# Kernel tuning notes

Hardware: AMD Instinct MI355X
Metric: run time of the kernel (lower is better)

Reference implementation:

```python
import jax, jax.numpy as jnp
import numpy as np

H = 16       # num_attention_heads
KV = 4       # num_key_value_heads
HD = 128     # head_dim
BASE = 10000.0


def rotate_half(x):
    x1, x2 = jnp.split(x, 2, axis=-1)
    return jnp.concatenate((-x2, x1), axis=-1)


def rope_cos_sin(position_ids):
    # inv_freq: (HD/2,)
    inv_freq = 1.0 / (BASE ** (jnp.arange(0, HD, 2, dtype=jnp.float32) / HD))
    freqs = position_ids.astype(jnp.float32)[..., None] * inv_freq  # (B, S, HD/2)
    emb = jnp.concatenate((freqs, freqs), axis=-1)  # (B, S, HD)
    return jnp.cos(emb), jnp.sin(emb)


def setup_inputs() -> dict:
    key = jax.random.key(0)
    ks = jax.random.split(key, 5)
    B, S, D = 2, 2048, 2048
    sc = 1.0 / np.sqrt(D)
    return {
        "hidden_states": jax.random.normal(ks[0], (B, S, D), jnp.float32),
        "position_ids": jnp.broadcast_to(jnp.arange(S, dtype=jnp.int32), (B, S)),
        "wq": jax.random.normal(ks[1], (H * HD, D), jnp.float32) * sc,
        "wk": jax.random.normal(ks[2], (KV * HD, D), jnp.float32) * sc,
        "wv": jax.random.normal(ks[3], (KV * HD, D), jnp.float32) * sc,
        "wo": jax.random.normal(ks[4], (H * HD, H * HD), jnp.float32) * sc,
    }


def attention_forward(hidden_states, position_ids, wq, wk, wv, wo):
    B, S, D = hidden_states.shape
    n_rep = H // KV
    # projections -> (B, heads, S, HD)
    q = (hidden_states @ wq.T).reshape(B, S, H, HD).transpose(0, 2, 1, 3)
    k = (hidden_states @ wk.T).reshape(B, S, KV, HD).transpose(0, 2, 1, 3)
    v = (hidden_states @ wv.T).reshape(B, S, KV, HD).transpose(0, 2, 1, 3)
    # RoPE
    cos, sin = rope_cos_sin(position_ids)  # (B, S, HD)
    cos = cos[:, None]  # (B, 1, S, HD)
    sin = sin[:, None]
    q = q * cos + rotate_half(q) * sin
    k = k * cos + rotate_half(k) * sin
    # repeat kv heads for GQA: (B, KV, S, HD) -> (B, H, S, HD)
    k = jnp.repeat(k, n_rep, axis=1)
    v = jnp.repeat(v, n_rep, axis=1)
    scale = 1.0 / np.sqrt(HD)
    scores = jnp.einsum("bhqd,bhkd->bhqk", q, k) * scale
    attn = jax.nn.softmax(scores.astype(jnp.float32), axis=-1).astype(q.dtype)
    out = jnp.einsum("bhqk,bhkd->bhqd", attn, v)
    out = out.transpose(0, 2, 1, 3).reshape(B, S, H * HD)
    return out @ wo.T


def reference(hidden_states, position_ids, wq, wk, wv, wo):
    return attention_forward(hidden_states, position_ids, wq, wk, wv, wo)
```

## Files before the change

### kernel.cpp

```cpp
#include <hip/hip_runtime.h>
#include <hip/hip_bf16.h>
#include <math.h>


typedef __attribute__((ext_vector_type(4))) float f32x4;
typedef __attribute__((ext_vector_type(8))) short short8;
typedef __attribute__((ext_vector_type(4))) unsigned short u16x4;
typedef __attribute__((ext_vector_type(8))) unsigned short u16x8;

static __device__ __forceinline__ unsigned short f2bf(float x) {
    unsigned u = __builtin_bit_cast(unsigned, x);
    u += 0x7fffu + ((u >> 16) & 1u);
    return (unsigned short)(u >> 16);
}
static __device__ __forceinline__ float bf2f(unsigned short h) {
    unsigned u = ((unsigned)h) << 16;
    return __builtin_bit_cast(float, u);
}
static __device__ __forceinline__ float exp2_fast(float x) {
    float r;
    asm volatile("v_exp_f32 %0, %1" : "=v"(r) : "v"(x));
    return r;
}
static __device__ __forceinline__ void gload16(const unsigned short* g, unsigned short* lds) {
    __builtin_amdgcn_global_load_lds((const __attribute__((address_space(1))) void*)g,
                                     (__attribute__((address_space(3))) void*)lds, 16, 0, 0);
}

__global__ __launch_bounds__(256) void k_conv(const float* __restrict__ src,
                                              unsigned short* __restrict__ dst, int n4) {
    int i = blockIdx.x * 256 + threadIdx.x;
    if (i >= n4) return;
    f32x4 v = ((const f32x4*)src)[i];
    u16x4 o;
    o.x = f2bf(v.x); o.y = f2bf(v.y); o.z = f2bf(v.z); o.w = f2bf(v.w);
    ((u16x4*)dst)[i] = o;
}

__global__ __launch_bounds__(256) void k_conv_wqkv(const float* __restrict__ wq,
                                                   const float* __restrict__ wk,
                                                   const float* __restrict__ wv,
                                                   unsigned short* __restrict__ dst) {
    int i = blockIdx.x * 256 + threadIdx.x;
    long flat = (long)i * 4;
    int row = (int)(flat >> 11);
    int col = (int)(flat & 2047);
    const float* src;
    if (row < 2560) {
        int base = row & 2047;
        int hh = base >> 7, ii = base & 127;
        int d = (ii >> 1) + ((ii & 1) << 6);
        src = (row < 2048 ? wq : wk) + (size_t)(hh * 128 + d) * 2048;
    } else {
        src = wv + (size_t)(row - 2560) * 2048;
    }
    f32x4 v = *(const f32x4*)(src + col);
    u16x4 o;
    o.x = f2bf(v.x); o.y = f2bf(v.y); o.z = f2bf(v.z); o.w = f2bf(v.w);
    *(u16x4*)(dst + flat) = o;
}

__global__ void k_rope_table(const int* __restrict__ pos_ids, float2* __restrict__ tb) {
    int r = blockIdx.x;
    int i = threadIdx.x;
    float pos = (float)pos_ids[r];
    float powv = (float)pow(10000.0, (double)i / 64.0);
    float invf = 1.0f / powv;
    float arg  = pos * invf;
    double a = (double)arg;
    tb[(size_t)r * 64 + i] = make_float2((float)cos(a), (float)sin(a));
}

template <int EPI>
__global__ __launch_bounds__(256) void k_gemm(const unsigned short* __restrict__ A,
                                              const unsigned short* __restrict__ W,
                                              float* __restrict__ Cf,
                                              unsigned short* __restrict__ qkvt,
                                              unsigned short* __restrict__ vtb,
                                              const float2* __restrict__ tb,
                                              int M, int N, int K) {
    __shared__ unsigned short As[2][4096];
    __shared__ unsigned short Ws[2][4096];
    const int tid = threadIdx.x;
    const int lane = tid & 63;
    const int w = tid >> 6;
    const int q = lane & 15, g = lane >> 4;
    const int wr = w >> 1, wc = w & 1;
    const long mbase = (long)blockIdx.y * 128;
    const long nbase = (long)blockIdx.x * 128;

    const unsigned short* gA[2];
    const unsigned short* gW[2];
    #pragma unroll
    for (int j = 0; j < 2; ++j) {
        int r = j * 64 + (tid >> 2);
        int slot = (tid & 3) ^ ((r >> 1) & 3);
        gA[j] = A + (size_t)(mbase + r) * K + slot * 8;
        gW[j] = W + (size_t)(nbase + r) * K + slot * 8;
    }
    const int sa = (g ^ ((q >> 1) & 3)) * 8;

    f32x4 acc[4][4];
    #pragma unroll
    for (int m = 0; m < 4; ++m)
        #pragma unroll
        for (int n = 0; n < 4; ++n) acc[m][n] = (f32x4){0.f, 0.f, 0.f, 0.f};

    auto STAGE = [&](int buf) {
        #pragma unroll
        for (int j = 0; j < 2; ++j) {
            gload16(gA[j], &As[buf][j * 2048 + w * 512]);
            gload16(gW[j], &Ws[buf][j * 2048 + w * 512]);
            gA[j] += 32; gW[j] += 32;
        }
    };

    const int nk = K >> 5;
    STAGE(0);
    int cur = 0;
    for (int t = 0; t < nk; ++t) {
        if (t) __builtin_amdgcn_s_barrier();
        if (t + 1 < nk) {
            STAGE(cur ^ 1);
            asm volatile("s_waitcnt vmcnt(4)" ::: "memory");
        } else {
            asm volatile("s_waitcnt vmcnt(0)" ::: "memory");
        }
        __builtin_amdgcn_s_barrier();

        short8 af[4], bfr[4];
        #pragma unroll
        for (int m = 0; m < 4; ++m) af[m] = *(const short8*)&As[cur][(wr * 64 + m * 16 + q) * 32 + sa];
        #pragma unroll
        for (int n = 0; n < 4; ++n) bfr[n] = *(const short8*)&Ws[cur][(wc * 64 + n * 16 + q) * 32 + sa];
        #pragma unroll
        for (int m = 0; m < 4; ++m)
            #pragma unroll
            for (int n = 0; n < 4; ++n)
                acc[m][n] = __builtin_amdgcn_mfma_f32_16x16x32_bf16(af[m], bfr[n], acc[m][n], 0, 0, 0);
        cur ^= 1;
    }

    if (EPI == 0) {
        #pragma unroll
        for (int m = 0; m < 4; ++m)
            #pragma unroll
            for (int n = 0; n < 4; ++n)
                #pragma unroll
                for (int rr = 0; rr < 4; ++rr) {
                    long row = mbase + wr * 64 + m * 16 + 4 * g + rr;
                    long col = nbase + wc * 64 + n * 16 + q;
                    Cf[row * N + col] = acc[m][n][rr];
                }
    } else {
        const int tile = blockIdx.x;
        if (tile >= 20) {
            const int kv = tile - 20;
            #pragma unroll
            for (int m = 0; m < 4; ++m)
                #pragma unroll
                for (int n = 0; n < 4; ++n) {
                    int c = wc * 64 + n * 16 + q;
                    long r0 = mbase + wr * 64 + m * 16 + 4 * g;
                    int b = (int)(r0 >> 11), s0 = (int)(r0 & 2047);
                    u16x4 pk;
                    #pragma unroll
                    for (int rr = 0; rr < 4; ++rr) pk[rr] = f2bf(acc[m][n][rr]);
                    *(u16x4*)(vtb + (size_t)((b * 4 + kv) * 128 + c) * 2048 + s0) = pk;
                }
        } else {
            const float scale = (tile < 16) ? 0.12751744f : 1.0f;
            const float sgn = (q & 1) ? 1.f : -1.f;
            #pragma unroll
            for (int m = 0; m < 4; ++m)
                #pragma unroll
                for (int rr = 0; rr < 4; ++rr) {
                    long row = mbase + wr * 64 + m * 16 + 4 * g + rr;
                    #pragma unroll
                    for (int n = 0; n < 4; ++n) {
                        int c = wc * 64 + n * 16 + q;
                        float x = acc[m][n][rr];
                        float p = __shfl_xor(x, 1);
                        float2 cs = tb[row * 64 + (c >> 1)];
                        float y = (x * cs.x + sgn * (p * cs.y)) * scale;
                        int dorig = (c >> 1) + ((c & 1) << 6);
                        long col = (tile < 16) ? (tile * 128 + dorig)
                                               : (2048 + (tile - 16) * 128 + dorig);
                        qkvt[row * 3072 + col] = f2bf(y);
                    }
                }
        }
    }
}

__global__ __launch_bounds__(256, 2) void k_flash(const unsigned short* __restrict__ qkv,
                                                  const unsigned short* __restrict__ vt,
                                                  unsigned short* __restrict__ aout) {
    __shared__ unsigned short Ks[2][8192];
    __shared__ unsigned short Vs[2][8192];
    __shared__ unsigned short Plds[4][1152];
    const int wg = blockIdx.x;
    const int kvg = wg & 7;
    const int inner = wg >> 3;
    const int h_in = inner & 3;
    const int qt = inner >> 2;
    const int b = kvg >> 2, kvh = kvg & 3;
    const int h = kvh * 4 + h_in;
    const int tid = threadIdx.x;
    const int w = tid >> 6, lane = tid & 63;
    const int q = lane & 15, g = lane >> 4;
    const int qrow = qt * 128 + w * 32;

    short8 qf[2][4];
    #pragma unroll
    for (int u = 0; u < 2; ++u) {
        const unsigned short* Qp = qkv + (size_t)(b * 2048 + qrow + u * 16 + q) * 3072 + h * 128 + g * 8;
        #pragma unroll
        for (int t = 0; t < 4; ++t) qf[u][t] = *(const short8*)(Qp + t * 32);
    }

    const unsigned short* Kbase = qkv + (size_t)(b * 2048) * 3072 + 2048 + kvh * 128;
    const unsigned short* Vbase = vt + (size_t)((b * 4 + kvh) * 128) * 2048;
    const unsigned short* gK[4];
    const unsigned short* gV[4];
    #pragma unroll
    for (int i = 0; i < 4; ++i) {
        int rowK = w * 16 + i * 4 + (lane >> 4);
        gK[i] = Kbase + (size_t)rowK * 3072 + (((lane & 15) ^ (rowK & 7)) << 3);
        int rowV = w * 32 + i * 8 + (lane >> 3);
        gV[i] = Vbase + (size_t)rowV * 2048 + (((lane & 7) ^ (rowV & 7)) << 3);
    }

    const int swz = (q & 7) << 3;
    int tcK[4];
    #pragma unroll
    for (int t = 0; t < 4; ++t) tcK[t] = (t * 32 + g * 8) ^ swz;

    unsigned short* Pw = Plds[w];

    float m_run[2] = {-INFINITY, -INFINITY};
    float l_run[2] = {0.f, 0.f};
    f32x4 o[2][8];
    #pragma unroll
    for (int u = 0; u < 2; ++u)
        #pragma unroll
        for (int nf = 0; nf < 8; ++nf) o[u][nf] = (f32x4){0.f, 0.f, 0.f, 0.f};

    auto STAGE = [&](int buf) {
        #pragma unroll
        for (int i = 0; i < 4; ++i) {
            gload16(gK[i], &Ks[buf][w * 2048 + i * 512]);
            gload16(gV[i], &Vs[buf][w * 2048 + i * 512]);
            gK[i] += 64 * 3072;
            gV[i] += 64;
        }
    };

    STAGE(0);
    int cur = 0;
    for (int t0 = 0; t0 < 32; ++t0) {
        if (t0 > 0) __builtin_amdgcn_s_barrier();
        if (t0 + 1 < 32) {
            STAGE(cur ^ 1);
            asm volatile("s_waitcnt vmcnt(8)" ::: "memory");
        } else {
            asm volatile("s_waitcnt vmcnt(0)" ::: "memory");
        }
        __builtin_amdgcn_s_barrier();

        const unsigned short* Kt = Ks[cur];
        const unsigned short* Vt = Vs[cur];

        f32x4 st[2][4];
        #pragma unroll
        for (int ks = 0; ks < 4; ++ks) {
            f32x4 a0 = (f32x4){0.f, 0.f, 0.f, 0.f};
            f32x4 a1 = (f32x4){0.f, 0.f, 0.f, 0.f};
            int rb = (ks * 16 + q) * 128;
            #pragma unroll
            for (int t = 0; t < 4; ++t) {
                short8 kf = *(const short8*)&Kt[rb + tcK[t]];
                a0 = __builtin_amdgcn_mfma_f32_16x16x32_bf16(kf, qf[0][t], a0, 0, 0, 0);
                a1 = __builtin_amdgcn_mfma_f32_16x16x32_bf16(kf, qf[1][t], a1, 0, 0, 0);
            }
            st[0][ks] = a0; st[1][ks] = a1;
        }

        short8 vf[8][2];
        #pragma unroll
        for (int nf = 0; nf < 8; ++nf) {
            int rb = (nf * 16 + q) * 64;
            #pragma unroll
            for (int t = 0; t < 2; ++t) vf[nf][t] = *(const short8*)&Vt[rb + tcK[t]];
        }

        #pragma unroll
        for (int u = 0; u < 2; ++u) {
            float mx = fmaxf(
                fmaxf(fmaxf(fmaxf(st[u][0][0], st[u][0][1]), fmaxf(st[u][0][2], st[u][0][3])),
                      fmaxf(fmaxf(st[u][1][0], st[u][1][1]), fmaxf(st[u][1][2], st[u][1][3]))),
                fmaxf(fmaxf(fmaxf(st[u][2][0], st[u][2][1]), fmaxf(st[u][2][2], st[u][2][3])),
                      fmaxf(fmaxf(st[u][3][0], st[u][3][1]), fmaxf(st[u][3][2], st[u][3][3]))));
            mx = fmaxf(mx, __shfl_xor(mx, 16));
            mx = fmaxf(mx, __shfl_xor(mx, 32));
            if (__any(mx - m_run[u] > 8.0f)) {
                float mn = fmaxf(m_run[u], mx);
                float sc = exp2_fast(m_run[u] - mn);
                l_run[u] *= sc;
                f32x4 sv;
                #pragma unroll
                for (int rr = 0; rr < 4; ++rr) sv[rr] = __shfl(sc, 4 * g + rr);
                #pragma unroll
                for (int nf = 0; nf < 8; ++nf) o[u][nf] *= sv;
                m_run[u] = mn;
            }
            f32x4 pe[4];
            #pragma unroll
            for (int ks = 0; ks < 4; ++ks)
                #pragma unroll
                for (int rr = 0; rr < 4; ++rr) pe[ks][rr] = exp2_fast(st[u][ks][rr] - m_run[u]);
            f32x4 ls4 = (pe[0] + pe[1]) + (pe[2] + pe[3]);
            float ls = (ls4[0] + ls4[1]) + (ls4[2] + ls4[3]);
            ls += __shfl_xor(ls, 16);
            ls += __shfl_xor(ls, 32);
            l_run[u] += ls;

            #pragma unroll
            for (int ks = 0; ks < 4; ++ks) {
                u16x4 pk;
                #pragma unroll
                for (int rr = 0; rr < 4; ++rr) pk[rr] = f2bf(pe[ks][rr]);
                *(u16x4*)&Pw[q * 72 + ks * 16 + 4 * g] = pk;
            }
            asm volatile("s_waitcnt lgkmcnt(0)" ::: "memory");
            short8 pa0 = *(const short8*)&Pw[q * 72 + g * 8];
            short8 pa1 = *(const short8*)&Pw[q * 72 + 32 + g * 8];

            #pragma unroll
            for (int nf = 0; nf < 8; ++nf) {
                f32x4 a = o[u][nf];
                a = __builtin_amdgcn_mfma_f32_16x16x32_bf16(pa0, vf[nf][0], a, 0, 0, 0);
                a = __builtin_amdgcn_mfma_f32_16x16x32_bf16(pa1, vf[nf][1], a, 0, 0, 0);
                o[u][nf] = a;
            }
        }
        cur ^= 1;
    }

    #pragma unroll
    for (int u = 0; u < 2; ++u) {
        f32x4 li;
        #pragma unroll
        for (int rr = 0; rr < 4; ++rr) li[rr] = __shfl(l_run[u], 4 * g + rr);
        #pragma unroll
        for (int nf = 0; nf < 8; ++nf)
            #pragma unroll
            for (int rr = 0; rr < 4; ++rr) {
                size_t row = (size_t)(b * 2048 + qrow + u * 16 + 4 * g + rr);
                aout[row * 2048 + h * 128 + nf * 16 + q] = f2bf(o[u][nf][rr] / li[rr]);
            }
    }
}

extern "C" void kernel_launch(void* const* d_in, const int* in_sizes, int n_in,
                              void* d_out, int out_size, void* d_ws, size_t ws_size,
                              hipStream_t stream) {
    (void)in_sizes; (void)n_in; (void)out_size; (void)ws_size;
    const float* hs = (const float*)d_in[0];
    const int* pos  = (const int*)d_in[1];
    const float* wq = (const float*)d_in[2];
    const float* wk = (const float*)d_in[3];
    const float* wv = (const float*)d_in[4];
    const float* wo = (const float*)d_in[5];
    float* out = (float*)d_out;

    unsigned short* hsb   = (unsigned short*)d_ws;
    unsigned short* wqkvb = hsb + (size_t)4096 * 2048;
    unsigned short* wob   = wqkvb + (size_t)3072 * 2048;
    unsigned short* qkvt  = wob + (size_t)2048 * 2048;
    unsigned short* vtb   = qkvt + (size_t)4096 * 3072;
    float2* tb            = (float2*)(vtb + (size_t)8 * 128 * 2048);
    unsigned short* aoutb = (unsigned short*)(tb + (size_t)4096 * 64);

    k_conv<<<8192, 256, 0, stream>>>(hs, hsb, 2097152);
    k_conv_wqkv<<<6144, 256, 0, stream>>>(wq, wk, wv, wqkvb);
    k_conv<<<4096, 256, 0, stream>>>(wo, wob, 1048576);
    k_rope_table<<<4096, 64, 0, stream>>>(pos, tb);
    k_gemm<1><<<dim3(24, 32), 256, 0, stream>>>(hsb, wqkvb, nullptr, qkvt, vtb, tb, 4096, 3072, 2048);
    k_flash<<<dim3(512), 256, 0, stream>>>(qkvt, vtb, aoutb);
    k_gemm<0><<<dim3(16, 32), 256, 0, stream>>>(aoutb, wob, out, nullptr, nullptr, nullptr, 4096, 2048, 2048);
}
```

Baseline: 233.2 us.

## Load V fragments directly from global memory in flash kernel and raise occupancy

The flash-attention kernel no longer stages V tiles through LDS. Each lane now reads its V fragments straight from the transposed V buffer in global memory, which halves LDS use so three workgroups can run per CU (launch bounds raised from 2 to 3). The change also wraps the MFMA sections in s_setprio, packs P to bf16 with the v_cvt_pk_bf16_f32 instruction, and multiplies by a reciprocal instead of dividing during the final normalisation. The direct V loads sit on the critical path with less latency hiding, which trades global/L2 traffic against the LDS savings.

```diff
diff --git a/kernel.cpp b/kernel.cpp
--- a/kernel.cpp
+++ b/kernel.cpp
@@ -20,6 +20,11 @@
 static __device__ __forceinline__ float exp2_fast(float x) {
     float r;
     asm volatile("v_exp_f32 %0, %1" : "=v"(r) : "v"(x));
+    return r;
+}
+static __device__ __forceinline__ unsigned cvt_pk_bf16(float a, float b) {
+    unsigned r;
+    asm("v_cvt_pk_bf16_f32 %0, %1, %2" : "=v"(r) : "v"(a), "v"(b));
     return r;
 }
 static __device__ __forceinline__ void gload16(const unsigned short* g, unsigned short* lds) {
@@ -193,11 +198,10 @@
     }
 }
 
-__global__ __launch_bounds__(256, 2) void k_flash(const unsigned short* __restrict__ qkv,
+__global__ __launch_bounds__(256, 3) void k_flash(const unsigned short* __restrict__ qkv,
                                                   const unsigned short* __restrict__ vt,
                                                   unsigned short* __restrict__ aout) {
     __shared__ unsigned short Ks[2][8192];
-    __shared__ unsigned short Vs[2][8192];
     __shared__ unsigned short Plds[4][1152];
     const int wg = blockIdx.x;
     const int kvg = wg & 7;
@@ -222,14 +226,12 @@
     const unsigned short* Kbase = qkv + (size_t)(b * 2048) * 3072 + 2048 + kvh * 128;
     const unsigned short* Vbase = vt + (size_t)((b * 4 + kvh) * 128) * 2048;
     const unsigned short* gK[4];
-    const unsigned short* gV[4];
     #pragma unroll
     for (int i = 0; i < 4; ++i) {
         int rowK = w * 16 + i * 4 + (lane >> 4);
         gK[i] = Kbase + (size_t)rowK * 3072 + (((lane & 15) ^ (rowK & 7)) << 3);
-        int rowV = w * 32 + i * 8 + (lane >> 3);
-        gV[i] = Vbase + (size_t)rowV * 2048 + (((lane & 7) ^ (rowV & 7)) << 3);
-    }
+    }
+    const unsigned short* Vp = Vbase + (size_t)q * 2048 + g * 8;
 
     const int swz = (q & 7) << 3;
     int tcK[4];
@@ -250,9 +252,7 @@
         #pragma unroll
         for (int i = 0; i < 4; ++i) {
             gload16(gK[i], &Ks[buf][w * 2048 + i * 512]);
-            gload16(gV[i], &Vs[buf][w * 2048 + i * 512]);
             gK[i] += 64 * 3072;
-            gV[i] += 64;
         }
     };
 
@@ -262,16 +262,24 @@
         if (t0 > 0) __builtin_amdgcn_s_barrier();
         if (t0 + 1 < 32) {
             STAGE(cur ^ 1);
-            asm volatile("s_waitcnt vmcnt(8)" ::: "memory");
+            asm volatile("s_waitcnt vmcnt(4)" ::: "memory");
         } else {
             asm volatile("s_waitcnt vmcnt(0)" ::: "memory");
         }
         __builtin_amdgcn_s_barrier();
 
         const unsigned short* Kt = Ks[cur];
-        const unsigned short* Vt = Vs[cur];
+
+        short8 vf[8][2];
+        #pragma unroll
+        for (int nf = 0; nf < 8; ++nf) {
+            const unsigned short* vp = Vp + (size_t)nf * 16 * 2048 + t0 * 64;
+            vf[nf][0] = *(const short8*)(vp);
+            vf[nf][1] = *(const short8*)(vp + 32);
+        }
 
         f32x4 st[2][4];
+        __builtin_amdgcn_s_setprio(1);
         #pragma unroll
         for (int ks = 0; ks < 4; ++ks) {
             f32x4 a0 = (f32x4){0.f, 0.f, 0.f, 0.f};
@@ -285,14 +293,7 @@
             }
             st[0][ks] = a0; st[1][ks] = a1;
         }
-
-        short8 vf[8][2];
-        #pragma unroll
-        for (int nf = 0; nf < 8; ++nf) {
-            int rb = (nf * 16 + q) * 64;
-            #pragma unroll
-            for (int t = 0; t < 2; ++t) vf[nf][t] = *(const short8*)&Vt[rb + tcK[t]];
-        }
+        __builtin_amdgcn_s_setprio(0);
 
         #pragma unroll
         for (int u = 0; u < 2; ++u) {
@@ -327,15 +328,16 @@
 
             #pragma unroll
             for (int ks = 0; ks < 4; ++ks) {
-                u16x4 pk;
-                #pragma unroll
-                for (int rr = 0; rr < 4; ++rr) pk[rr] = f2bf(pe[ks][rr]);
-                *(u16x4*)&Pw[q * 72 + ks * 16 + 4 * g] = pk;
+                uint2 pk;
+                pk.x = cvt_pk_bf16(pe[ks][0], pe[ks][1]);
+                pk.y = cvt_pk_bf16(pe[ks][2], pe[ks][3]);
+                *(uint2*)&Pw[q * 72 + ks * 16 + 4 * g] = pk;
             }
             asm volatile("s_waitcnt lgkmcnt(0)" ::: "memory");
             short8 pa0 = *(const short8*)&Pw[q * 72 + g * 8];
             short8 pa1 = *(const short8*)&Pw[q * 72 + 32 + g * 8];
 
+            __builtin_amdgcn_s_setprio(1);
             #pragma unroll
             for (int nf = 0; nf < 8; ++nf) {
                 f32x4 a = o[u][nf];
@@ -343,21 +345,24 @@
                 a = __builtin_amdgcn_mfma_f32_16x16x32_bf16(pa1, vf[nf][1], a, 0, 0, 0);
                 o[u][nf] = a;
             }
+            __builtin_amdgcn_s_setprio(0);
         }
         cur ^= 1;
     }
 
     #pragma unroll
     for (int u = 0; u < 2; ++u) {
-        f32x4 li;
+        f32x4 li, li_inv;
         #pragma unroll
         for (int rr = 0; rr < 4; ++rr) li[rr] = __shfl(l_run[u], 4 * g + rr);
+        #pragma unroll
+        for (int rr = 0; rr < 4; ++rr) li_inv[rr] = 1.0f / li[rr];
         #pragma unroll
         for (int nf = 0; nf < 8; ++nf)
             #pragma unroll
             for (int rr = 0; rr < 4; ++rr) {
                 size_t row = (size_t)(b * 2048 + qrow + u * 16 + 4 * g + rr);
-                aout[row * 2048 + h * 128 + nf * 16 + q] = f2bf(o[u][nf][rr] / li[rr]);
+                aout[row * 2048 + h * 128 + nf * 16 + q] = f2bf(o[u][nf][rr] * li_inv[rr]);
             }
     }
 }
```

After: 558.7 us. 2.4x slower.

## Fuse conversion and RoPE-table kernels into one prep launch; swizzle GEMM tile order

Applied to the files above, without the earlier changes.

Merges the three bf16 conversion kernels and the RoPE table kernel into a single k_prep launch that picks its work by flat index range, removing three launches and the gaps between them. It also remaps GEMM block IDs with an XCD-aware swizzle so that consecutive blocks on the same chiplet share A/W tiles in L2. The QKV epilogue now uses the swizzled column tile index. The fused kernel has divergent branches at range boundaries, and the RoPE part now runs 256-thread blocks instead of 64.

```diff
diff --git a/kernel.cpp b/kernel.cpp
--- a/kernel.cpp
+++ b/kernel.cpp
@@ -27,48 +27,57 @@
                                      (__attribute__((address_space(3))) void*)lds, 16, 0, 0);
 }
 
-__global__ __launch_bounds__(256) void k_conv(const float* __restrict__ src,
-                                              unsigned short* __restrict__ dst, int n4) {
-    int i = blockIdx.x * 256 + threadIdx.x;
-    if (i >= n4) return;
-    f32x4 v = ((const f32x4*)src)[i];
-    u16x4 o;
-    o.x = f2bf(v.x); o.y = f2bf(v.y); o.z = f2bf(v.z); o.w = f2bf(v.w);
-    ((u16x4*)dst)[i] = o;
-}
-
-__global__ __launch_bounds__(256) void k_conv_wqkv(const float* __restrict__ wq,
-                                                   const float* __restrict__ wk,
-                                                   const float* __restrict__ wv,
-                                                   unsigned short* __restrict__ dst) {
-    int i = blockIdx.x * 256 + threadIdx.x;
-    long flat = (long)i * 4;
-    int row = (int)(flat >> 11);
-    int col = (int)(flat & 2047);
-    const float* src;
-    if (row < 2560) {
-        int base = row & 2047;
-        int hh = base >> 7, ii = base & 127;
-        int d = (ii >> 1) + ((ii & 1) << 6);
-        src = (row < 2048 ? wq : wk) + (size_t)(hh * 128 + d) * 2048;
+__global__ __launch_bounds__(256) void k_prep(const float* __restrict__ hs,
+                                              const float* __restrict__ wq,
+                                              const float* __restrict__ wk,
+                                              const float* __restrict__ wv,
+                                              const float* __restrict__ wo,
+                                              const int* __restrict__ pos_ids,
+                                              unsigned short* __restrict__ hsb,
+                                              unsigned short* __restrict__ wqkvb,
+                                              unsigned short* __restrict__ wob,
+                                              float2* __restrict__ tb) {
+    long idx = (long)blockIdx.x * 256 + threadIdx.x;
+    if (idx < 2097152) {
+        f32x4 v = ((const f32x4*)hs)[idx];
+        u16x4 o;
+        o.x = f2bf(v.x); o.y = f2bf(v.y); o.z = f2bf(v.z); o.w = f2bf(v.w);
+        ((u16x4*)hsb)[idx] = o;
+    } else if (idx < 3670016) {
+        long i = idx - 2097152;
+        long flat = i * 4;
+        int row = (int)(flat >> 11);
+        int col = (int)(flat & 2047);
+        const float* src;
+        if (row < 2560) {
+            int base = row & 2047;
+            int hh = base >> 7, ii = base & 127;
+            int d = (ii >> 1) + ((ii & 1) << 6);
+            src = (row < 2048 ? wq : wk) + (size_t)(hh * 128 + d) * 2048;
+        } else {
+            src = wv + (size_t)(row - 2560) * 2048;
+        }
+        f32x4 v = *(const f32x4*)(src + col);
+        u16x4 o;
+        o.x = f2bf(v.x); o.y = f2bf(v.y); o.z = f2bf(v.z); o.w = f2bf(v.w);
+        *(u16x4*)(wqkvb + flat) = o;
+    } else if (idx < 4718592) {
+        long i = idx - 3670016;
+        f32x4 v = ((const f32x4*)wo)[i];
+        u16x4 o;
+        o.x = f2bf(v.x); o.y = f2bf(v.y); o.z = f2bf(v.z); o.w = f2bf(v.w);
+        ((u16x4*)wob)[i] = o;
     } else {
-        src = wv + (size_t)(row - 2560) * 2048;
-    }
-    f32x4 v = *(const f32x4*)(src + col);
-    u16x4 o;
-    o.x = f2bf(v.x); o.y = f2bf(v.y); o.z = f2bf(v.z); o.w = f2bf(v.w);
-    *(u16x4*)(dst + flat) = o;
-}
-
-__global__ void k_rope_table(const int* __restrict__ pos_ids, float2* __restrict__ tb) {
-    int r = blockIdx.x;
-    int i = threadIdx.x;
-    float pos = (float)pos_ids[r];
-    float powv = (float)pow(10000.0, (double)i / 64.0);
-    float invf = 1.0f / powv;
-    float arg  = pos * invf;
-    double a = (double)arg;
-    tb[(size_t)r * 64 + i] = make_float2((float)cos(a), (float)sin(a));
+        long j = idx - 4718592;
+        int r = (int)(j >> 6);
+        int i = (int)(j & 63);
+        float pos = (float)pos_ids[r];
+        float powv = (float)pow(10000.0, (double)i / 64.0);
+        float invf = 1.0f / powv;
+        float arg  = pos * invf;
+        double a = (double)arg;
+        tb[(size_t)r * 64 + i] = make_float2((float)cos(a), (float)sin(a));
+    }
 }
 
 template <int EPI>
@@ -86,8 +95,14 @@
     const int w = tid >> 6;
     const int q = lane & 15, g = lane >> 4;
     const int wr = w >> 1, wc = w & 1;
-    const long mbase = (long)blockIdx.y * 128;
-    const long nbase = (long)blockIdx.x * 128;
+
+    const int nwg = gridDim.x * gridDim.y;
+    const int id = blockIdx.y * gridDim.x + blockIdx.x;
+    const int swz_id = (id & 7) * (nwg >> 3) + (id >> 3);
+    const int bx = swz_id % gridDim.x;
+    const int by = swz_id / gridDim.x;
+    const long mbase = (long)by * 128;
+    const long nbase = (long)bx * 128;
 
     const unsigned short* gA[2];
     const unsigned short* gW[2];
@@ -153,7 +168,7 @@
                     Cf[row * N + col] = acc[m][n][rr];
                 }
     } else {
-        const int tile = blockIdx.x;
+        const int tile = bx;
         if (tile >= 20) {
             const int kv = tile - 20;
             #pragma unroll
@@ -382,10 +397,7 @@
     float2* tb            = (float2*)(vtb + (size_t)8 * 128 * 2048);
     unsigned short* aoutb = (unsigned short*)(tb + (size_t)4096 * 64);
 
-    k_conv<<<8192, 256, 0, stream>>>(hs, hsb, 2097152);
-    k_conv_wqkv<<<6144, 256, 0, stream>>>(wq, wk, wv, wqkvb);
-    k_conv<<<4096, 256, 0, stream>>>(wo, wob, 1048576);
-    k_rope_table<<<4096, 64, 0, stream>>>(pos, tb);
+    k_prep<<<19456, 256, 0, stream>>>(hs, wq, wk, wv, wo, pos, hsb, wqkvb, wob, tb);
     k_gemm<1><<<dim3(24, 32), 256, 0, stream>>>(hsb, wqkvb, nullptr, qkvt, vtb, tb, 4096, 3072, 2048);
     k_flash<<<dim3(512), 256, 0, stream>>>(qkvt, vtb, aoutb);
     k_gemm<0><<<dim3(16, 32), 256, 0, stream>>>(aoutb, wob, out, nullptr, nullptr, nullptr, 4096, 2048, 2048);
```

Result: faster. 226.5 us (-2.8%).
